# Optimization experiments

Measured on AMD Instinct MI355X. Metric: run time of the kernel, lower is better.

## Reference

```python
import jax, jax.numpy as jnp
import numpy as np

B, S, D, H = 2, 2048, 1024, 16
DK = D // H
LN_EPS = 1e-5


def setup_inputs() -> dict:
    key = jax.random.key(0)
    ks = jax.random.split(key, 10)
    scale = 1.0 / np.sqrt(D)
    return {
        "input_Q": jax.random.normal(ks[0], (B, S, D), jnp.float32),
        "input_K": jax.random.normal(ks[1], (B, S, D), jnp.float32),
        "input_V": jax.random.normal(ks[2], (B, S, D), jnp.float32),
        "mask": jax.random.randint(ks[3], (B, S, S), 0, 2, jnp.int32),
        "W_Q": jax.random.normal(ks[4], (D, D), jnp.float32) * scale,
        "W_K": jax.random.normal(ks[5], (D, D), jnp.float32) * scale,
        "W_V": jax.random.normal(ks[6], (D, D), jnp.float32) * scale,
        "W_O": jax.random.normal(ks[7], (D, D), jnp.float32) * scale,
        "ln_gamma": jnp.ones((D,), jnp.float32),
        "ln_beta": jnp.zeros((D,), jnp.float32),
    }


def reference(input_Q, input_K, input_V, mask, W_Q, W_K, W_V, W_O, ln_gamma, ln_beta):
    # projections -> [B, H, S, DK]
    q = (input_Q @ W_Q).reshape(B, S, H, DK).transpose(0, 2, 1, 3)
    k = (input_K @ W_K).reshape(B, S, H, DK).transpose(0, 2, 1, 3)
    v = (input_V @ W_V).reshape(B, S, H, DK).transpose(0, 2, 1, 3)

    # explicit O(S^2) scores as in the original module
    scores = jnp.einsum("bhqd,bhkd->bhqk", q, k) / np.sqrt(DK)
    scores = jnp.where(mask[:, None, :, :].astype(bool), -1e9, scores)
    attn = jax.nn.softmax(scores, axis=-1)
    ctx = jnp.einsum("bhqk,bhkd->bhqd", attn, v)

    # merge heads, output projection, residual + LayerNorm
    ctx = ctx.transpose(0, 2, 1, 3).reshape(B, S, D)
    out = ctx @ W_O + input_Q
    mu = out.mean(-1, keepdims=True)
    var = jnp.mean((out - mu) ** 2, -1, keepdims=True)
    return (out - mu) * jax.lax.rsqrt(var + LN_EPS) * ln_gamma + ln_beta
```

## Files before the change

kernel.cpp:

```cpp
#include <hip/hip_runtime.h>

typedef __bf16 bf16x8 __attribute__((ext_vector_type(8)));
typedef float  f32x4  __attribute__((ext_vector_type(4)));
typedef short  s16x2  __attribute__((ext_vector_type(2)));

#define AS1 __attribute__((address_space(1)))
#define AS3 __attribute__((address_space(3)))

__device__ __forceinline__ void g2l16(const void* g, void* l) {
  __builtin_amdgcn_global_load_lds((AS1 void*)g, (AS3 void*)l, 16, 0, 0);
}
#define MFMA16(a, b, c) __builtin_amdgcn_mfma_f32_16x16x32_bf16(a, b, c, 0, 0, 0)

__device__ __forceinline__ unsigned pack_bf16(float a, float b) {
  union { __bf16 h[2]; unsigned u; } p;
  p.h[0] = (__bf16)a; p.h[1] = (__bf16)b;
  return p.u;
}

__global__ __launch_bounds__(256) void prep(const float* __restrict__ inQ,
    const float* __restrict__ inK, const float* __restrict__ inV,
    const int* __restrict__ mask,
    const float* __restrict__ W0, const float* __restrict__ W1,
    const float* __restrict__ W2, const float* __restrict__ W3,
    __bf16* __restrict__ Xq, __bf16* __restrict__ Xk, __bf16* __restrict__ Xv,
    unsigned long long* __restrict__ bits, __bf16* __restrict__ Wt) {
  __shared__ __bf16 tile[64][65];
  const int blk = blockIdx.x;
  if (blk < 6144) {
    const int z = blk >> 11, bx = blk & 2047;
    const float* src = z == 0 ? inQ : (z == 1 ? inK : inV);
    __bf16* dst = z == 0 ? Xq : (z == 1 ? Xk : Xv);
    size_t base = ((size_t)bx * 256 + threadIdx.x) * 8;
    float4 f0 = *(const float4*)(src + base);
    float4 f1 = *(const float4*)(src + base + 4);
    bf16x8 o;
    o[0] = (__bf16)f0.x; o[1] = (__bf16)f0.y; o[2] = (__bf16)f0.z; o[3] = (__bf16)f0.w;
    o[4] = (__bf16)f1.x; o[5] = (__bf16)f1.y; o[6] = (__bf16)f1.z; o[7] = (__bf16)f1.w;
    *(bf16x8*)(dst + base) = o;
  } else if (blk < 10240) {
    const int lane = threadIdx.x & 63, w = threadIdx.x >> 6;
    const int base = (blk - 6144) * 2048 + w * 512;
#pragma unroll
    for (int it = 0; it < 8; ++it) {
      int i = base + it * 64 + lane;
      unsigned long long bb = __ballot(mask[i] == 0);
      if (lane == 0) bits[i >> 6] = bb;
    }
  } else {
    const int idx = blk - 10240;
    const int z = idx >> 8, rem = idx & 255, bx = rem & 15, by = rem >> 4;
    const float* srcs[4] = {W0, W1, W2, W3};
    const float* src = srcs[z];
    __bf16* dst = Wt + (size_t)z * 1024 * 1024;
    int cb = bx * 64, rb = by * 64;
    for (int i = threadIdx.x; i < 4096; i += 256) {
      int r = i >> 6, c = i & 63;
      tile[r][c] = (__bf16)src[(size_t)(rb + r) * 1024 + cb + c];
    }
    __syncthreads();
    for (int i = threadIdx.x; i < 4096; i += 256) {
      int c = i >> 6, r = i & 63;
      dst[(size_t)(cb + c) * 1024 + rb + r] = tile[r][c];
    }
  }
}

__global__ __launch_bounds__(256) void qkv_gemm(const __bf16* __restrict__ Xq,
    const __bf16* __restrict__ Xk, const __bf16* __restrict__ Xv,
    const __bf16* __restrict__ Wt, __bf16* __restrict__ Qb,
    __bf16* __restrict__ Kb, __bf16* __restrict__ Vtb) {
  __shared__ __align__(16) __bf16 sh[8192];
  __bf16* As = sh;
  __bf16* Bs = sh + 4096;
  const int z = blockIdx.z;
  const __bf16* X = z == 0 ? Xq : (z == 1 ? Xk : Xv);
  const __bf16* W = Wt + (size_t)z * 1048576;
  const float scale = z == 0 ? 0.125f * 1.44269504088896f : 1.f;
  const int t = threadIdx.x;
  const int lane = t & 63, w = t >> 6;
  const int lane15 = lane & 15, quad = lane >> 4;
  const int wm = (w >> 1) * 64, wn = (w & 1) * 64;
  const int mBase = blockIdx.y * 128, nBase = blockIdx.x * 128;
  const int c1 = t, c2 = t + 256;
  f32x4 acc[4][4] = {};
  for (int kt = 0; kt < 1024; kt += 32) {
    __syncthreads();
    g2l16(X + (size_t)(mBase + (c1 >> 2)) * 1024 + kt + (c1 & 3) * 8, As + c1 * 8);
    g2l16(X + (size_t)(mBase + (c2 >> 2)) * 1024 + kt + (c2 & 3) * 8, As + c2 * 8);
    g2l16(W + (size_t)(nBase + (c1 >> 2)) * 1024 + kt + (c1 & 3) * 8, Bs + c1 * 8);
    g2l16(W + (size_t)(nBase + (c2 >> 2)) * 1024 + kt + (c2 & 3) * 8, Bs + c2 * 8);
    __builtin_amdgcn_s_waitcnt(0);
    __syncthreads();
    bf16x8 a[4], b[4];
#pragma unroll
    for (int i = 0; i < 4; i++) a[i] = *(const bf16x8*)&As[(wm + i * 16 + lane15) * 32 + quad * 8];
#pragma unroll
    for (int j = 0; j < 4; j++) b[j] = *(const bf16x8*)&Bs[(wn + j * 16 + lane15) * 32 + quad * 8];
#pragma unroll
    for (int i = 0; i < 4; i++)
#pragma unroll
      for (int j = 0; j < 4; j++)
        acc[i][j] = MFMA16(a[i], b[j], acc[i][j]);
  }
  if (z != 2) {
    __bf16* Y = z == 0 ? Qb : Kb;
#pragma unroll
    for (int i = 0; i < 4; i++)
#pragma unroll
      for (int j = 0; j < 4; j++)
#pragma unroll
        for (int r = 0; r < 4; r++) {
          int mg = mBase + wm + i * 16 + quad * 4 + r;
          int ng = nBase + wn + j * 16 + lane15;
          int b_ = mg >> 11, s_ = mg & 2047, h_ = ng >> 6, d_ = ng & 63;
          Y[(((size_t)(b_ * 16 + h_)) * 2048 + s_) * 64 + d_] = (__bf16)(acc[i][j][r] * scale);
        }
  } else {
    const int s0 = mBase & 2047;
    const int bhBase = (mBase >> 11) * 16 + (nBase >> 6);
#pragma unroll
    for (int half = 0; half < 2; ++half) {
      __syncthreads();
      if ((w & 1) == half) {
#pragma unroll
        for (int i = 0; i < 4; i++)
#pragma unroll
          for (int j = 0; j < 4; j++)
#pragma unroll
            for (int r = 0; r < 4; r++) {
              int nl = j * 16 + lane15;
              int ml = wm + i * 16 + quad * 4 + r;
              int l5 = ml & 31;
              int mlp = (ml & 96) | ((((l5 >> 2) & 3) * 8) + ((l5 & 3) * 2) + ((l5 >> 4) & 1));
              sh[nl * 128 + (mlp ^ ((nl & 7) * 16))] = (__bf16)acc[i][j][r];
            }
      }
      __syncthreads();
      const int row = t >> 2, c0 = (t & 3) * 32;
      const int xr = (row & 7) * 16;
      const int b0 = row * 128 + (c0 ^ xr);
      const int b1 = row * 128 + ((c0 + 16) ^ xr);
      bf16x8 a0 = *(const bf16x8*)&sh[b0];
      bf16x8 a1 = *(const bf16x8*)&sh[b0 + 8];
      bf16x8 a2 = *(const bf16x8*)&sh[b1];
      bf16x8 a3 = *(const bf16x8*)&sh[b1 + 8];
      __bf16* dst = Vtb + (size_t)(bhBase + half) * 131072 + (size_t)row * 2048 + s0 + c0;
      *(bf16x8*)(dst)      = a0;
      *(bf16x8*)(dst + 8)  = a1;
      *(bf16x8*)(dst + 16) = a2;
      *(bf16x8*)(dst + 24) = a3;
    }
  }
}

__global__ __launch_bounds__(256) void gemm_wo(const __bf16* __restrict__ X,
    const __bf16* __restrict__ Wt, const float* __restrict__ resid,
    float* __restrict__ Yf) {
  __shared__ __align__(16) __bf16 As[64 * 32];
  __shared__ __align__(16) __bf16 Bs[128 * 32];
  const int t = threadIdx.x;
  const int lane = t & 63, w = t >> 6;
  const int lane15 = lane & 15, quad = lane >> 4;
  const int wm = (w >> 1) * 32, wn = (w & 1) * 64;
  const int mBase = blockIdx.y * 64, nBase = blockIdx.x * 128;
  f32x4 acc[2][4] = {};
  for (int kt = 0; kt < 1024; kt += 32) {
    __syncthreads();
    g2l16(X  + (size_t)(mBase + (t >> 2)) * 1024 + kt + (t & 3) * 8, As + t * 8);
    g2l16(Wt + (size_t)(nBase + (t >> 2)) * 1024 + kt + (t & 3) * 8, Bs + t * 8);
    g2l16(Wt + (size_t)(nBase + ((t + 256) >> 2)) * 1024 + kt + (t & 3) * 8, Bs + (t + 256) * 8);
    __builtin_amdgcn_s_waitcnt(0);
    __syncthreads();
    bf16x8 a[2], b[4];
#pragma unroll
    for (int i = 0; i < 2; i++) a[i] = *(const bf16x8*)&As[(wm + i * 16 + lane15) * 32 + quad * 8];
#pragma unroll
    for (int j = 0; j < 4; j++) b[j] = *(const bf16x8*)&Bs[(wn + j * 16 + lane15) * 32 + quad * 8];
#pragma unroll
    for (int i = 0; i < 2; i++)
#pragma unroll
      for (int j = 0; j < 4; j++)
        acc[i][j] = MFMA16(a[i], b[j], acc[i][j]);
  }
#pragma unroll
  for (int i = 0; i < 2; i++)
#pragma unroll
    for (int j = 0; j < 4; j++)
#pragma unroll
      for (int r = 0; r < 4; r++) {
        int mg = mBase + wm + i * 16 + quad * 4 + r;
        int ng = nBase + wn + j * 16 + lane15;
        size_t idx = (size_t)mg * 1024 + ng;
        Yf[idx] = acc[i][j][r] + resid[idx];
      }
}

__global__ __launch_bounds__(256, 4) void attn_kernel(const __bf16* __restrict__ Q,
    const __bf16* __restrict__ Kp, const __bf16* __restrict__ Vt,
    const unsigned* __restrict__ mbits, __bf16* __restrict__ ctx) {
  __shared__ __align__(16) __bf16 Qs[64 * 64];
  __shared__ __align__(16) __bf16 Ks[4][32 * 64];
  __shared__ __align__(16) __bf16 Vs[4][64 * 32];
  const int t = threadIdx.x, lane = t & 63, w = t >> 6;
  const int l15 = lane & 15, quad = lane >> 4;
  const int id = blockIdx.x + (blockIdx.y << 5);
  const int iix = id >> 3;
  const int bh = (id & 7) * 4 + (iix >> 5);
  const int qBase = (iix & 31) * 64;
  const int b = bh >> 4, h = bh & 15;
  const size_t qko = (size_t)bh * 2048 * 64;
  const size_t vko = (size_t)bh * 64 * 2048;
  const int srow8 = lane >> 3, sch8 = (lane & 7) ^ srow8;
  const int srow16 = lane >> 2, sch4 = (lane & 3) ^ ((lane >> 3) & 3);
  const int stOff = w * 512 + lane * 8;
  const __bf16* kSrc = Kp + qko + (size_t)(w * 8 + srow8) * 64 + sch8 * 8;
  const __bf16* vSrc = Vt + vko + (size_t)(w * 16 + srow16) * 2048 + sch4 * 8;
  __bf16* KsF = &Ks[0][0];
  __bf16* VsF = &Vs[0][0];
  g2l16(Q + qko + (size_t)(qBase + w * 8 + srow8) * 64 + sch8 * 8,       Qs + w * 512 + lane * 8);
  g2l16(Q + qko + (size_t)(qBase + (w + 4) * 8 + srow8) * 64 + sch8 * 8, Qs + (w + 4) * 512 + lane * 8);
  g2l16(kSrc,        KsF + stOff);
  g2l16(vSrc,        VsF + stOff);
  g2l16(kSrc + 2048, KsF + 2048 + stOff);
  g2l16(vSrc + 32,   VsF + 2048 + stOff);
  const __bf16* kStage = kSrc + 2 * 2048;
  const __bf16* vStage = vSrc + 2 * 32;
  const size_t mIdx = ((size_t)b * 2048 + qBase + w * 16 + l15) * 64;
  unsigned mCur = mbits[mIdx];
  unsigned mPrev = 0;
  __builtin_amdgcn_s_waitcnt(0);
  __syncthreads();
  bf16x8 qb0, qb1;
  {
    const int r = w * 16 + l15, s = r & 7;
    qb0 = *(const bf16x8*)&Qs[r * 64 + ((quad ^ s) * 8)];
    qb1 = *(const bf16x8*)&Qs[r * 64 + (((4 + quad) ^ s) * 8)];
  }
  const int sA = l15 & 7, trB = 16 + l15, sB = trB & 7;
  const __bf16* pKA0 = KsF + l15 * 64 + ((quad ^ sA) * 8);
  const __bf16* pKA1 = KsF + l15 * 64 + (((4 + quad) ^ sA) * 8);
  const __bf16* pKB0 = KsF + trB * 64 + ((quad ^ sB) * 8);
  const __bf16* pKB1 = KsF + trB * 64 + (((4 + quad) ^ sB) * 8);
  const int dr0 = l15,      dr1 = 16 + l15, dr2 = 32 + l15, dr3 = 48 + l15;
  const __bf16* pV0 = VsF + dr0 * 32 + ((quad ^ ((dr0 >> 1) & 3)) * 8);
  const __bf16* pV1 = VsF + dr1 * 32 + ((quad ^ ((dr1 >> 1) & 3)) * 8);
  const __bf16* pV2 = VsF + dr2 * 32 + ((quad ^ ((dr2 >> 1) & 3)) * 8);
  const __bf16* pV3 = VsF + dr3 * 32 + ((quad ^ ((dr3 >> 1) & 3)) * 8);
  bf16x8 krA[2][2], krB[2][2];
  krA[0][0] = *(const bf16x8*)(pKA0);
  krA[0][1] = *(const bf16x8*)(pKA1);
  krA[1][0] = *(const bf16x8*)(pKB0);
  krA[1][1] = *(const bf16x8*)(pKB1);
  bf16x8 ones;
#pragma unroll
  for (int i = 0; i < 8; i++) ones[i] = (__bf16)1.0f;
  f32x4 o[4] = {};
  f32x4 ol = {};
  f32x4 stA[2] = {}, stB[2] = {};
  bf16x8 paA = {}, paB = {};
  bf16x8 vrA[4] = {}, vrB[4] = {};

#define ATTN_BODY(KT, SLS, SLK, SLV, KC, KN, STO, STI, PAO, PAI, VRO, VRI)          \
  {                                                                                 \
    __syncthreads();                 \
    if ((KT) < 62) {                                                                \
      g2l16(kStage, KsF + (SLS) * 2048 + stOff); kStage += 2048;                    \
      g2l16(vStage, VsF + (SLS) * 2048 + stOff); vStage += 32;                      \
    }                                                                               \
    unsigned mNew = 0;                                                              \
    if ((KT) < 63) mNew = mbits[mIdx + (KT) + 1];                                   \
                \
    __builtin_amdgcn_s_setprio(1);                                                  \
    {                                                                               \
      f32x4 zz = {0.f, 0.f, 0.f, 0.f};                                              \
      zz     = MFMA16(KC[0][0], qb0, zz);                                           \
      STO[0] = MFMA16(KC[0][1], qb1, zz);                                           \
      f32x4 zy = {0.f, 0.f, 0.f, 0.f};                                              \
      zy     = MFMA16(KC[1][0], qb0, zy);                                           \
      STO[1] = MFMA16(KC[1][1], qb1, zy);                                           \
    }                                                                               \
                                  \
    if ((KT) >= 2) {                                                                \
      ol   = MFMA16(PAI, ones,   ol);                                               \
      o[0] = MFMA16(PAI, VRI[0], o[0]);                                             \
      o[1] = MFMA16(PAI, VRI[1], o[1]);                                             \
      o[2] = MFMA16(PAI, VRI[2], o[2]);                                             \
      o[3] = MFMA16(PAI, VRI[3], o[3]);                                             \
    }                                                                               \
    __builtin_amdgcn_s_setprio(0);                                                  \
                    \
    if ((KT) < 63) {                                                                \
      KN[0][0] = *(const bf16x8*)(pKA0 + (SLK) * 2048);                             \
      KN[0][1] = *(const bf16x8*)(pKA1 + (SLK) * 2048);                             \
      KN[1][0] = *(const bf16x8*)(pKB0 + (SLK) * 2048);                             \
      KN[1][1] = *(const bf16x8*)(pKB1 + (SLK) * 2048);                             \
    }                                                                               \
                    \
    if ((KT) >= 1) {                                                                \
      VRO[0] = *(const bf16x8*)(pV0 + (SLV) * 2048);                                \
      VRO[1] = *(const bf16x8*)(pV1 + (SLV) * 2048);                                \
      VRO[2] = *(const bf16x8*)(pV2 + (SLV) * 2048);                                \
      VRO[3] = *(const bf16x8*)(pV3 + (SLV) * 2048);                                \
    }                                                                               \
        \
    if ((KT) >= 1) {                                                                \
      const unsigned msh = mPrev >> (quad * 4);                                     \
      union { unsigned u[4]; bf16x8 v; } pk;                                        \
      _Pragma("unroll")                                                             \
      for (int r = 0; r < 4; r++) {                                                 \
        float e0 = __builtin_amdgcn_exp2f(STI[0][r]);                               \
        float e1 = __builtin_amdgcn_exp2f(STI[1][r]);                               \
        union { unsigned u; s16x2 s; } mc;                                          \
        mc.u = msh << (15 - r);                                                     \
        mc.s = mc.s >> 15;                                                          \
        pk.u[r] = pack_bf16(e0, e1) & mc.u;                                         \
      }                                                                             \
      PAO = pk.v;                                                                   \
    }                                                                               \
    mPrev = mCur; mCur = mNew;                                                      \
  }

  for (int kt = 0; kt < 64; kt += 4) {
    ATTN_BODY(kt + 0, 2, 1, 3, krA, krB, stA, stB, paB, paA, vrB, vrA);
    ATTN_BODY(kt + 1, 3, 2, 0, krB, krA, stB, stA, paA, paB, vrA, vrB);
    ATTN_BODY(kt + 2, 0, 3, 1, krA, krB, stA, stB, paB, paA, vrB, vrA);
    ATTN_BODY(kt + 3, 1, 0, 2, krB, krA, stB, stA, paA, paB, vrA, vrB);
  }
#undef ATTN_BODY

  {
    vrB[0] = *(const bf16x8*)(pV0 + 3 * 2048);
    vrB[1] = *(const bf16x8*)(pV1 + 3 * 2048);
    vrB[2] = *(const bf16x8*)(pV2 + 3 * 2048);
    vrB[3] = *(const bf16x8*)(pV3 + 3 * 2048);
    __builtin_amdgcn_s_setprio(1);
    ol   = MFMA16(paA, ones,   ol);
    o[0] = MFMA16(paA, vrA[0], o[0]);
    o[1] = MFMA16(paA, vrA[1], o[1]);
    o[2] = MFMA16(paA, vrA[2], o[2]);
    o[3] = MFMA16(paA, vrA[3], o[3]);
    __builtin_amdgcn_s_setprio(0);
    const unsigned msh = mPrev >> (quad * 4);
    union { unsigned u[4]; bf16x8 v; } pk;
#pragma unroll
    for (int r = 0; r < 4; r++) {
      float e0 = __builtin_amdgcn_exp2f(stB[0][r]);
      float e1 = __builtin_amdgcn_exp2f(stB[1][r]);
      union { unsigned u; s16x2 s; } mc;
      mc.u = msh << (15 - r);
      mc.s = mc.s >> 15;
      pk.u[r] = pack_bf16(e0, e1) & mc.u;
    }
    paB = pk.v;
    __builtin_amdgcn_s_setprio(1);
    ol   = MFMA16(paB, ones,   ol);
    o[0] = MFMA16(paB, vrB[0], o[0]);
    o[1] = MFMA16(paB, vrB[1], o[1]);
    o[2] = MFMA16(paB, vrB[2], o[2]);
    o[3] = MFMA16(paB, vrB[3], o[3]);
    __builtin_amdgcn_s_setprio(0);
  }
#pragma unroll
  for (int r = 0; r < 4; r++) {
    float inv = 1.f / ol[r];
    int qg = qBase + w * 16 + quad * 4 + r;
    size_t base = ((size_t)b * 2048 + qg) * 1024 + h * 64;
#pragma unroll
    for (int j = 0; j < 4; j++)
      ctx[base + j * 16 + l15] = (__bf16)(o[j][r] * inv);
  }
}

__global__ __launch_bounds__(256) void ln_kernel(const float* __restrict__ X,
    const float* __restrict__ gamma, const float* __restrict__ beta,
    float* __restrict__ out) {
  __shared__ float red[8];
  const int t = threadIdx.x;
  const size_t row = blockIdx.x;
  const float* xr = X + row * 1024;
  float4 x = *(const float4*)(xr + t * 4);
  float s = x.x + x.y + x.z + x.w;
  float s2 = x.x * x.x + x.y * x.y + x.z * x.z + x.w * x.w;
#pragma unroll
  for (int off = 1; off < 64; off <<= 1) { s += __shfl_xor(s, off); s2 += __shfl_xor(s2, off); }
  if ((t & 63) == 0) { red[t >> 6] = s; red[4 + (t >> 6)] = s2; }
  __syncthreads();
  float S1 = red[0] + red[1] + red[2] + red[3];
  float S2 = red[4] + red[5] + red[6] + red[7];
  float mu = S1 * (1.f / 1024.f);
  float var = S2 * (1.f / 1024.f) - mu * mu;
  float rs = rsqrtf(var + 1e-5f);
  float4 g = *(const float4*)(gamma + t * 4);
  float4 bb = *(const float4*)(beta + t * 4);
  float4 y;
  y.x = (x.x - mu) * rs * g.x + bb.x;
  y.y = (x.y - mu) * rs * g.y + bb.y;
  y.z = (x.z - mu) * rs * g.z + bb.z;
  y.w = (x.w - mu) * rs * g.w + bb.w;
  *(float4*)(out + row * 1024 + t * 4) = y;
}

extern "C" void kernel_launch(void* const* d_in, const int* in_sizes, int n_in,
                              void* d_out, int out_size, void* d_ws, size_t ws_size,
                              hipStream_t stream) {
  const float* inQ  = (const float*)d_in[0];
  const float* inK  = (const float*)d_in[1];
  const float* inV  = (const float*)d_in[2];
  const int*   mask = (const int*)d_in[3];
  const float* WQ   = (const float*)d_in[4];
  const float* WK   = (const float*)d_in[5];
  const float* WV   = (const float*)d_in[6];
  const float* WO   = (const float*)d_in[7];
  const float* gamma = (const float*)d_in[8];
  const float* beta  = (const float*)d_in[9];

  const size_t MB = 1024 * 1024;
  char* ws = (char*)d_ws;
  __bf16* Xq  = (__bf16*)(ws);
  __bf16* Xk  = (__bf16*)(ws + 8 * MB);
  __bf16* Xv  = (__bf16*)(ws + 16 * MB);
  __bf16* Qb  = (__bf16*)(ws + 24 * MB);
  __bf16* Kb  = (__bf16*)(ws + 32 * MB);
  __bf16* Vtb = (__bf16*)(ws + 48 * MB);
  __bf16* Wt  = (__bf16*)(ws + 56 * MB);
  unsigned long long* mbits = (unsigned long long*)(ws + 64 * MB);
  __bf16* ctx  = Xq;
  float*  outp = (float*)(ws + 8 * MB);

  prep<<<dim3(11264), 256, 0, stream>>>(inQ, inK, inV, mask, WQ, WK, WV, WO,
                                        Xq, Xk, Xv, mbits, Wt);
  qkv_gemm<<<dim3(8, 32, 3), 256, 0, stream>>>(Xq, Xk, Xv, Wt, Qb, Kb, Vtb);
  attn_kernel<<<dim3(32, 32), 256, 0, stream>>>(Qb, Kb, Vtb, (const unsigned*)mbits, ctx);
  gemm_wo<<<dim3(8, 64), 256, 0, stream>>>(ctx, Wt + 3 * 1048576, inQ, outp);
  ln_kernel<<<dim3(4096), 256, 0, stream>>>(outp, gamma, beta, (float*)d_out);
}
```

Baseline: 257.9 us.

## Double K-tile depth to 64 with XOR-swizzled LDS and grouped tile order in GEMMs

Both projection GEMMs now stage a K-slice of 64 instead of 32 per barrier pair. This halves the number of sync and wait points per output tile. LDS rows are XOR-swizzled on 16-byte chunks to avoid bank conflicts on the wider rows. Block indices are remapped into a grouped order so that neighbouring blocks share weight and activation tiles in L2. The cost is twice the LDS per block, which may reduce occupancy, and the loads are still not double-buffered.

```diff
diff --git a/kernel.cpp b/kernel.cpp
--- a/kernel.cpp
+++ b/kernel.cpp
@@ -70,9 +70,9 @@
     const __bf16* __restrict__ Xk, const __bf16* __restrict__ Xv,
     const __bf16* __restrict__ Wt, __bf16* __restrict__ Qb,
     __bf16* __restrict__ Kb, __bf16* __restrict__ Vtb) {
-  __shared__ __align__(16) __bf16 sh[8192];
+  __shared__ __align__(16) __bf16 sh[16384];
   __bf16* As = sh;
-  __bf16* Bs = sh + 4096;
+  __bf16* Bs = sh + 8192;
   const int z = blockIdx.z;
   const __bf16* X = z == 0 ? Xq : (z == 1 ? Xk : Xv);
   const __bf16* W = Wt + (size_t)z * 1048576;
@@ -81,27 +81,40 @@
   const int lane = t & 63, w = t >> 6;
   const int lane15 = lane & 15, quad = lane >> 4;
   const int wm = (w >> 1) * 64, wn = (w & 1) * 64;
-  const int mBase = blockIdx.y * 128, nBase = blockIdx.x * 128;
-  const int c1 = t, c2 = t + 256;
+  const int gid = blockIdx.x + (blockIdx.y << 3);
+  const int mt = (gid & 7) * 4 + ((gid >> 3) & 3);
+  const int nt = gid >> 5;
+  const int mBase = mt * 128, nBase = nt * 128;
+  const int xsw = lane15 & 7;
   f32x4 acc[4][4] = {};
-  for (int kt = 0; kt < 1024; kt += 32) {
+  for (int kt = 0; kt < 1024; kt += 64) {
     __syncthreads();
-    g2l16(X + (size_t)(mBase + (c1 >> 2)) * 1024 + kt + (c1 & 3) * 8, As + c1 * 8);
-    g2l16(X + (size_t)(mBase + (c2 >> 2)) * 1024 + kt + (c2 & 3) * 8, As + c2 * 8);
-    g2l16(W + (size_t)(nBase + (c1 >> 2)) * 1024 + kt + (c1 & 3) * 8, Bs + c1 * 8);
-    g2l16(W + (size_t)(nBase + (c2 >> 2)) * 1024 + kt + (c2 & 3) * 8, Bs + c2 * 8);
+#pragma unroll
+    for (int k4 = 0; k4 < 4; ++k4) {
+      const int c = t + 256 * k4;
+      const int gr = c >> 3, cc = c & 7;
+      const int so = ((cc ^ (gr & 7)) * 8);
+      g2l16(X + (size_t)(mBase + gr) * 1024 + kt + so, As + c * 8);
+      g2l16(W + (size_t)(nBase + gr) * 1024 + kt + so, Bs + c * 8);
+    }
     __builtin_amdgcn_s_waitcnt(0);
     __syncthreads();
-    bf16x8 a[4], b[4];
-#pragma unroll
-    for (int i = 0; i < 4; i++) a[i] = *(const bf16x8*)&As[(wm + i * 16 + lane15) * 32 + quad * 8];
-#pragma unroll
-    for (int j = 0; j < 4; j++) b[j] = *(const bf16x8*)&Bs[(wn + j * 16 + lane15) * 32 + quad * 8];
-#pragma unroll
-    for (int i = 0; i < 4; i++)
+#pragma unroll
+    for (int kk = 0; kk < 64; kk += 32) {
+      const int cb = kk >> 3;
+      bf16x8 a[4], b[4];
+#pragma unroll
+      for (int i = 0; i < 4; i++)
+        a[i] = *(const bf16x8*)&As[(wm + i * 16 + lane15) * 64 + (((cb + quad) ^ xsw) * 8)];
 #pragma unroll
       for (int j = 0; j < 4; j++)
-        acc[i][j] = MFMA16(a[i], b[j], acc[i][j]);
+        b[j] = *(const bf16x8*)&Bs[(wn + j * 16 + lane15) * 64 + (((cb + quad) ^ xsw) * 8)];
+#pragma unroll
+      for (int i = 0; i < 4; i++)
+#pragma unroll
+        for (int j = 0; j < 4; j++)
+          acc[i][j] = MFMA16(a[i], b[j], acc[i][j]);
+    }
   }
   if (z != 2) {
     __bf16* Y = z == 0 ? Qb : Kb;
@@ -157,31 +170,52 @@
 __global__ __launch_bounds__(256) void gemm_wo(const __bf16* __restrict__ X,
     const __bf16* __restrict__ Wt, const float* __restrict__ resid,
     float* __restrict__ Yf) {
-  __shared__ __align__(16) __bf16 As[64 * 32];
-  __shared__ __align__(16) __bf16 Bs[128 * 32];
+  __shared__ __align__(16) __bf16 As[64 * 64];
+  __shared__ __align__(16) __bf16 Bs[128 * 64];
   const int t = threadIdx.x;
   const int lane = t & 63, w = t >> 6;
   const int lane15 = lane & 15, quad = lane >> 4;
   const int wm = (w >> 1) * 32, wn = (w & 1) * 64;
-  const int mBase = blockIdx.y * 64, nBase = blockIdx.x * 128;
+  const int gid = blockIdx.x + (blockIdx.y << 3);
+  const int mt = (gid & 7) * 8 + ((gid >> 3) & 7);
+  const int nt = gid >> 6;
+  const int mBase = mt * 64, nBase = nt * 128;
+  const int xsw = lane15 & 7;
   f32x4 acc[2][4] = {};
-  for (int kt = 0; kt < 1024; kt += 32) {
+  for (int kt = 0; kt < 1024; kt += 64) {
     __syncthreads();
-    g2l16(X  + (size_t)(mBase + (t >> 2)) * 1024 + kt + (t & 3) * 8, As + t * 8);
-    g2l16(Wt + (size_t)(nBase + (t >> 2)) * 1024 + kt + (t & 3) * 8, Bs + t * 8);
-    g2l16(Wt + (size_t)(nBase + ((t + 256) >> 2)) * 1024 + kt + (t & 3) * 8, Bs + (t + 256) * 8);
+#pragma unroll
+    for (int k2 = 0; k2 < 2; ++k2) {
+      const int c = t + 256 * k2;
+      const int gr = c >> 3, cc = c & 7;
+      const int so = ((cc ^ (gr & 7)) * 8);
+      g2l16(X + (size_t)(mBase + gr) * 1024 + kt + so, As + c * 8);
+    }
+#pragma unroll
+    for (int k4 = 0; k4 < 4; ++k4) {
+      const int c = t + 256 * k4;
+      const int gr = c >> 3, cc = c & 7;
+      const int so = ((cc ^ (gr & 7)) * 8);
+      g2l16(Wt + (size_t)(nBase + gr) * 1024 + kt + so, Bs + c * 8);
+    }
     __builtin_amdgcn_s_waitcnt(0);
     __syncthreads();
-    bf16x8 a[2], b[4];
-#pragma unroll
-    for (int i = 0; i < 2; i++) a[i] = *(const bf16x8*)&As[(wm + i * 16 + lane15) * 32 + quad * 8];
-#pragma unroll
-    for (int j = 0; j < 4; j++) b[j] = *(const bf16x8*)&Bs[(wn + j * 16 + lane15) * 32 + quad * 8];
-#pragma unroll
-    for (int i = 0; i < 2; i++)
+#pragma unroll
+    for (int kk = 0; kk < 64; kk += 32) {
+      const int cb = kk >> 3;
+      bf16x8 a[2], b[4];
+#pragma unroll
+      for (int i = 0; i < 2; i++)
+        a[i] = *(const bf16x8*)&As[(wm + i * 16 + lane15) * 64 + (((cb + quad) ^ xsw) * 8)];
 #pragma unroll
       for (int j = 0; j < 4; j++)
-        acc[i][j] = MFMA16(a[i], b[j], acc[i][j]);
+        b[j] = *(const bf16x8*)&Bs[(wn + j * 16 + lane15) * 64 + (((cb + quad) ^ xsw) * 8)];
+#pragma unroll
+      for (int i = 0; i < 2; i++)
+#pragma unroll
+        for (int j = 0; j < 4; j++)
+          acc[i][j] = MFMA16(a[i], b[j], acc[i][j]);
+    }
   }
 #pragma unroll
   for (int i = 0; i < 2; i++)
```

New measurement: 262.9 us. No clear change (+1.9%).
